# Optimization experiments

Measured on AMD Instinct MI355X. Metric: run time of the kernel, lower is better.

The kernel has to match this reference:

```python
import jax, jax.numpy as jnp
import numpy as np

N, D, H, B_GRAPHS = 200000, 512, 64, 512


def setup_inputs() -> dict:
    key = jax.random.key(0)
    k1, k2, k3, k4, k5, k6 = jax.random.split(key, 6)
    x = jax.random.normal(k1, (N, D), dtype=jnp.float32)
    batch = jnp.sort(jax.random.randint(k2, (N,), 0, B_GRAPHS, dtype=jnp.int64))
    # attn MLP params: Linear(D,64) -> Tanh -> Linear(64,1)
    s1 = 1.0 / np.sqrt(D)
    s2 = 1.0 / np.sqrt(H)
    W1 = jax.random.uniform(k3, (D, H), jnp.float32, -s1, s1)
    b1 = jax.random.uniform(k4, (H,), jnp.float32, -s1, s1)
    W2 = jax.random.uniform(k5, (H, 1), jnp.float32, -s2, s2)
    b2 = jax.random.uniform(k6, (1,), jnp.float32, -s2, s2)
    return {"x": x, "W1": W1, "b1": b1, "W2": W2, "b2": b2, "batch": batch, "B": B_GRAPHS}


def reference(x, W1, b1, W2, b2, batch, B):
    # scorer MLP: (N,D) -> (N,1)
    scores = jnp.tanh(x @ W1 + b1) @ W2 + b2  # (N,1)
    s = scores[:, 0]  # (N,)
    # segment softmax over nodes grouped by graph id (pyg_softmax semantics)
    seg_max = jax.ops.segment_max(s, batch, num_segments=B)  # (B,)
    seg_max = jnp.where(jnp.isfinite(seg_max), seg_max, 0.0)  # guard empty segments
    e = jnp.exp(s - seg_max[batch])  # (N,)
    denom = jax.ops.segment_sum(e, batch, num_segments=B)  # (B,)
    w = e / (denom[batch] + 1e-16)  # (N,) attention weights
    # weighted scatter-add of node embeddings -> graph embeddings
    out = jax.ops.segment_sum(x * w[:, None], batch, num_segments=B)  # (B,D)
    return out
```

## Files before the change

### kernel.cpp

```cpp
#include <hip/hip_runtime.h>
#include <hip/hip_bf16.h>
#include <math.h>

#define TD 512
#define TH 64
#define CHUNK 16
#define NT 256

typedef __attribute__((ext_vector_type(8))) short bf16x8;
typedef __attribute__((ext_vector_type(4))) float f32x4;

__device__ __forceinline__ unsigned short f2b(float f) {
    return __builtin_bit_cast(unsigned short, __float2bfloat16(f));
}

__device__ __forceinline__ float tanh_fast(float v) {
    float e = __expf(2.0f * v);
    return 1.0f - 2.0f / (e + 1.0f);
}

__device__ __forceinline__ void barrier_lgkm() {
    asm volatile("s_waitcnt lgkmcnt(0)" ::: "memory");
    __builtin_amdgcn_s_barrier();
}

template <int CTRL>
__device__ __forceinline__ float dpp_add(float v) {
    int r = __builtin_amdgcn_update_dpp(0, __builtin_bit_cast(int, v), CTRL, 0xf, 0xf, false);
    return v + __builtin_bit_cast(float, r);
}
__device__ __forceinline__ float row16_sum(float v) {
    v = dpp_add<0x121>(v);
    v = dpp_add<0x122>(v);
    v = dpp_add<0x124>(v);
    v = dpp_add<0x128>(v);
    return v;
}

__global__ void prep_kernel(const int* __restrict__ batch32,
                            const float* __restrict__ W1,
                            int* __restrict__ off,
                            unsigned short* __restrict__ W1B,
                            int N, int B) {
    int i = blockIdx.x * blockDim.x + threadIdx.x;
    if (i < TH * TD) {
        int c = i >> 9;
        int k = i & 511;
        W1B[i] = f2b(W1[k * TH + c]);
    }
    if (i >= N) return;
    const bool is64 = (batch32[N - 1] == 0);
    auto bval = [&](int kk) -> int { return is64 ? batch32[2 * kk] : batch32[kk]; };
    int bc = bval(i);
    if (i == 0) {
        for (int j = 0; j <= bc; ++j) off[j] = 0;
    } else {
        int bp = bval(i - 1);
        for (int j = bp + 1; j <= bc; ++j) off[j] = i;
    }
    if (i == N - 1) {
        for (int j = bc + 1; j <= B; ++j) off[j] = N;
    }
}

__global__ __launch_bounds__(NT)
__attribute__((amdgpu_waves_per_eu(2, 2)))
void attnpool_kernel(const float* __restrict__ x,
                     const unsigned short* __restrict__ W1B,
                     const float* __restrict__ b1,
                     const float* __restrict__ W2,
                     const float* __restrict__ b2,
                     const int* __restrict__ off,
                     float* __restrict__ out,
                     int N)
{
    __shared__ __align__(16) char smem[TH * TD * 2];
    __shared__ float sP[4][CHUNK];
    __shared__ float wbuf[CHUNK];
    __shared__ float lsum;
    unsigned short* W1T  = (unsigned short*)smem;
    unsigned short* Atile = (unsigned short*)smem;

    const int tid  = threadIdx.x;
    const int b    = blockIdx.x;
    const int lane = tid & 63;
    const int ct   = tid >> 6;

    const int seg_start = off[b];
    const int seg_len   = off[b + 1] - seg_start;
    const float b2v = b2[0];

    const int rowcls = tid >> 7;
    const int col4   = (tid & 127) << 2;

    const int jcol = (ct << 4) + (lane & 15);
    const int kb   = (lane >> 4) << 3;
    const float b1v = b1[jcol];
    const float w2v = W2[jcol];

    float4 accw; accw.x = 0.f; accw.y = 0.f; accw.z = 0.f; accw.w = 0.f;
    float l_part = 0.0f;
    float4 xrA[8], xrB[8];

    auto load_chunk = [&](float4 (&xr)[8], int c0) {
        #pragma unroll
        for (int p = 0; p < 8; ++p) {
            int rl = (p << 1) + rowcls;
            int r  = c0 + rl;
            int gr = (r < seg_len) ? (seg_start + r) : seg_start;
            xr[p] = *reinterpret_cast<const float4*>(&x[(size_t)gr * TD + col4]);
        }
    };

    if (seg_len > 0) load_chunk(xrA, 0);

    {
        const bf16x8* W1B8 = reinterpret_cast<const bf16x8*>(W1B);
        #pragma unroll
        for (int i = 0; i < (TH * TD / 8) / NT; ++i) {
            int e8 = tid + NT * i;
            int c  = e8 >> 6;
            int k8 = e8 & 63;
            bf16x8 v = W1B8[e8];
            *reinterpret_cast<bf16x8*>(&W1T[(c * TD + (k8 << 3)) ^ ((c & 7) << 3)]) = v;
        }
    }
    barrier_lgkm();

    bf16x8 w1f[16];
    #pragma unroll
    for (int kk = 0; kk < 16; ++kk) {
        w1f[kk] = *reinterpret_cast<const bf16x8*>(
            &W1T[(jcol * TD + (kk << 5) + kb) ^ ((jcol & 7) << 3)]);
    }
    barrier_lgkm();

    auto body = [&](float4 (&cur)[8], float4 (&nxt)[8], int c0) {
        if (c0 + CHUNK < seg_len) load_chunk(nxt, c0 + CHUNK);

        #pragma unroll
        for (int p = 0; p < 8; ++p) {
            int rl = (p << 1) + rowcls;
            ushort4 v;
            v.x = f2b(cur[p].x); v.y = f2b(cur[p].y);
            v.z = f2b(cur[p].z); v.w = f2b(cur[p].w);
            *reinterpret_cast<ushort4*>(&Atile[(rl * TD + col4) ^ ((rl & 7) << 3)]) = v;
        }
        barrier_lgkm();

        f32x4 acc = {0, 0, 0, 0};
        const int rA = lane & 15;
        #pragma unroll
        for (int kk = 0; kk < 16; ++kk) {
            int k0 = (kk << 5) + kb;
            bf16x8 av = *reinterpret_cast<const bf16x8*>(
                &Atile[(rA * TD + k0) ^ ((rA & 7) << 3)]);
            acc = __builtin_amdgcn_mfma_f32_16x16x32_bf16(av, w1f[kk], acc, 0, 0, 0);
        }

        {
            float pv[4];
            #pragma unroll
            for (int q = 0; q < 4; ++q)
                pv[q] = row16_sum(tanh_fast(acc[q] + b1v) * w2v);
            if ((lane & 15) == 0) {
                int g = lane >> 4;
                #pragma unroll
                for (int q = 0; q < 4; ++q)
                    sP[ct][(g << 2) + q] = pv[q];
            }
        }
        barrier_lgkm();

        if (ct == 0 && lane < CHUNK) {
            float s = sP[0][lane] + sP[1][lane] + sP[2][lane] + sP[3][lane] + b2v;
            float e = ((c0 + lane) < seg_len) ? __expf(s) : 0.0f;
            wbuf[lane] = e;
            l_part += e;
        }
        barrier_lgkm();

        #pragma unroll
        for (int p = 0; p < 8; ++p) {
            float wgt = wbuf[(p << 1) + rowcls];
            accw.x += wgt * cur[p].x;
            accw.y += wgt * cur[p].y;
            accw.z += wgt * cur[p].z;
            accw.w += wgt * cur[p].w;
        }
    };

    if (seg_len > 0) {
        int c0 = 0;
        while (true) {
            body(xrA, xrB, c0);
            c0 += CHUNK;
            if (c0 >= seg_len) break;
            body(xrB, xrA, c0);
            c0 += CHUNK;
            if (c0 >= seg_len) break;
        }
    }

    float* fs = reinterpret_cast<float*>(Atile);
    __syncthreads();
    *reinterpret_cast<float4*>(&fs[rowcls * TD + col4]) = accw;
    if (ct == 0) {
        float ls = l_part;
        #pragma unroll
        for (int m = 1; m < 64; m <<= 1) ls += __shfl_xor(ls, m, 64);
        if (lane == 0) lsum = ls;
    }
    __syncthreads();
    float inv = 1.0f / (lsum + 1e-16f);
    out[(size_t)b * TD + tid]       = (fs[tid] + fs[TD + tid]) * inv;
    out[(size_t)b * TD + 256 + tid] = (fs[256 + tid] + fs[TD + 256 + tid]) * inv;
}

extern "C" void kernel_launch(void* const* d_in, const int* in_sizes, int n_in,
                              void* d_out, int out_size, void* d_ws, size_t ws_size,
                              hipStream_t stream) {
    const float* x  = (const float*)d_in[0];
    const float* W1 = (const float*)d_in[1];
    const float* b1 = (const float*)d_in[2];
    const float* W2 = (const float*)d_in[3];
    const float* b2 = (const float*)d_in[4];
    const int* batch = (const int*)d_in[5];
    int N = in_sizes[5];
    int B = out_size / TD;
    if (B <= 0 || N <= 0) return;

    int* off = (int*)d_ws;
    unsigned short* W1B = (unsigned short*)((char*)d_ws + 4096);

    int prep_elems = (N > TH * TD) ? N : TH * TD;
    prep_kernel<<<dim3((prep_elems + 255) / 256), dim3(256), 0, stream>>>(
        batch, W1, off, W1B, N, B);
    attnpool_kernel<<<dim3(B), dim3(NT), 0, stream>>>(
        x, W1B, b1, W2, b2, off, (float*)d_out, N);
}
```

Measured before the change: 87.51 us.

## Process 32-row chunks with two MFMA accumulators and shuffle-broadcast weights

Doubles the per-iteration chunk from 16 to 32 rows. Each wave now issues two MFMAs per k-step, reusing the W1 fragments, and the x register prefetch doubles. The wbuf shared-memory stage and its extra barrier are removed: every wave computes the exp weights redundantly and broadcasts them with __shfl. This cuts barriers and loop iterations per row but doubles register use for the prefetch buffers (32 float4) and increases padding waste on short segments. There is also a risk that the Atile region no longer fits or aliases correctly.

```diff
diff --git a/kernel.cpp b/kernel.cpp
--- a/kernel.cpp
+++ b/kernel.cpp
@@ -4,7 +4,7 @@
 
 #define TD 512
 #define TH 64
-#define CHUNK 16
+#define CHUNK 32
 #define NT 256
 
 typedef __attribute__((ext_vector_type(8))) short bf16x8;
@@ -76,9 +76,8 @@
 {
     __shared__ __align__(16) char smem[TH * TD * 2];
     __shared__ float sP[4][CHUNK];
-    __shared__ float wbuf[CHUNK];
     __shared__ float lsum;
-    unsigned short* W1T  = (unsigned short*)smem;
+    unsigned short* W1T   = (unsigned short*)smem;
     unsigned short* Atile = (unsigned short*)smem;
 
     const int tid  = threadIdx.x;
@@ -100,11 +99,11 @@
 
     float4 accw; accw.x = 0.f; accw.y = 0.f; accw.z = 0.f; accw.w = 0.f;
     float l_part = 0.0f;
-    float4 xrA[8], xrB[8];
-
-    auto load_chunk = [&](float4 (&xr)[8], int c0) {
-        #pragma unroll
-        for (int p = 0; p < 8; ++p) {
+    float4 xrA[16], xrB[16];
+
+    auto load_chunk = [&](float4 (&xr)[16], int c0) {
+        #pragma unroll
+        for (int p = 0; p < 16; ++p) {
             int rl = (p << 1) + rowcls;
             int r  = c0 + rl;
             int gr = (r < seg_len) ? (seg_start + r) : seg_start;
@@ -135,11 +134,11 @@
     }
     barrier_lgkm();
 
-    auto body = [&](float4 (&cur)[8], float4 (&nxt)[8], int c0) {
+    auto body = [&](float4 (&cur)[16], float4 (&nxt)[16], int c0) {
         if (c0 + CHUNK < seg_len) load_chunk(nxt, c0 + CHUNK);
 
         #pragma unroll
-        for (int p = 0; p < 8; ++p) {
+        for (int p = 0; p < 16; ++p) {
             int rl = (p << 1) + rowcls;
             ushort4 v;
             v.x = f2b(cur[p].x); v.y = f2b(cur[p].y);
@@ -148,41 +147,49 @@
         }
         barrier_lgkm();
 
-        f32x4 acc = {0, 0, 0, 0};
+        f32x4 acc0 = {0,0,0,0}, acc1 = {0,0,0,0};
         const int rA = lane & 15;
+        const int rB = rA + 16;
         #pragma unroll
         for (int kk = 0; kk < 16; ++kk) {
             int k0 = (kk << 5) + kb;
-            bf16x8 av = *reinterpret_cast<const bf16x8*>(
+            bf16x8 a0 = *reinterpret_cast<const bf16x8*>(
                 &Atile[(rA * TD + k0) ^ ((rA & 7) << 3)]);
-            acc = __builtin_amdgcn_mfma_f32_16x16x32_bf16(av, w1f[kk], acc, 0, 0, 0);
+            bf16x8 a1 = *reinterpret_cast<const bf16x8*>(
+                &Atile[(rB * TD + k0) ^ ((rB & 7) << 3)]);
+            acc0 = __builtin_amdgcn_mfma_f32_16x16x32_bf16(a0, w1f[kk], acc0, 0, 0, 0);
+            acc1 = __builtin_amdgcn_mfma_f32_16x16x32_bf16(a1, w1f[kk], acc1, 0, 0, 0);
         }
 
         {
-            float pv[4];
+            float pa[4], pb[4];
             #pragma unroll
-            for (int q = 0; q < 4; ++q)
-                pv[q] = row16_sum(tanh_fast(acc[q] + b1v) * w2v);
+            for (int q = 0; q < 4; ++q) {
+                pa[q] = row16_sum(tanh_fast(acc0[q] + b1v) * w2v);
+                pb[q] = row16_sum(tanh_fast(acc1[q] + b1v) * w2v);
+            }
             if ((lane & 15) == 0) {
                 int g = lane >> 4;
                 #pragma unroll
-                for (int q = 0; q < 4; ++q)
-                    sP[ct][(g << 2) + q] = pv[q];
+                for (int q = 0; q < 4; ++q) {
+                    sP[ct][(g << 2) + q]      = pa[q];
+                    sP[ct][16 + (g << 2) + q] = pb[q];
+                }
             }
         }
         barrier_lgkm();
 
-        if (ct == 0 && lane < CHUNK) {
-            float s = sP[0][lane] + sP[1][lane] + sP[2][lane] + sP[3][lane] + b2v;
-            float e = ((c0 + lane) < seg_len) ? __expf(s) : 0.0f;
-            wbuf[lane] = e;
-            l_part += e;
-        }
-        barrier_lgkm();
-
-        #pragma unroll
-        for (int p = 0; p < 8; ++p) {
-            float wgt = wbuf[(p << 1) + rowcls];
+        float ev;
+        {
+            int r = lane & 31;
+            float s = sP[0][r] + sP[1][r] + sP[2][r] + sP[3][r] + b2v;
+            ev = ((c0 + r) < seg_len) ? __expf(s) : 0.0f;
+            if (ct == 0 && lane < CHUNK) l_part += ev;
+        }
+
+        #pragma unroll
+        for (int p = 0; p < 16; ++p) {
+            float wgt = __shfl(ev, (p << 1) + rowcls, 64);
             accw.x += wgt * cur[p].x;
             accw.y += wgt * cur[p].y;
             accw.z += wgt * cur[p].z;
```

After: 212.1 us. 142% more time.
